# Optimization experiments

Hardware: AMD Instinct MI355X
Metric: run time of the kernel (lower is better)

Reference implementation:

```python
import jax, jax.numpy as jnp
import numpy as np

N_SCALES = 4
WINDOW = 64
REDUCTION = 4
EPS = 5e-05


def conv3x3_reflect(x, w):
    # reflect pad 1 then VALID 3x3 conv (no bias), NCHW/OIHW
    xp = jnp.pad(x, ((0, 0), (0, 0), (1, 1), (1, 1)), mode='reflect')
    return jax.lax.conv_general_dilated(
        xp, w, window_strides=(1, 1), padding='VALID',
        dimension_numbers=('NCHW', 'OIHW', 'NCHW'))


def add_adjacent_clusters(x):
    # x: (N, u, k, w, e); concat rolled-back and rolled-forward clusters on window axis
    x_back = jnp.roll(x, 1, axis=2)
    x_fwd = jnp.roll(x, -1, axis=2)
    return jnp.concatenate([x, x_back, x_fwd], axis=3)


def setup_inputs() -> dict:
    key = jax.random.key(0)
    ks = jax.random.split(key, 6)
    N, Cin, H, W = 2, 200, 128, 128
    inp = {
        'input': jax.random.normal(ks[0], (N, Cin, H, W), dtype=jnp.float32),
        'semantic_label': jax.random.randint(ks[1], (N, N_SCALES, H, W), 0, 32, dtype=jnp.int32),
        'Wx': jax.random.normal(ks[2], (Cin // REDUCTION, Cin, 3, 3), dtype=jnp.float32) * 0.02,
        'Wy': jax.random.normal(ks[3], (Cin, Cin, 1, 1), dtype=jnp.float32) * 0.02,
        'Wout': jax.random.normal(ks[4], (Cin, Cin * N_SCALES, 1, 1), dtype=jnp.float32) * 0.02,
        'bout': jax.random.normal(ks[5], (Cin,), dtype=jnp.float32) * 0.02,
    }
    return inp


def reference(input, semantic_label, Wx, Wy, Wout, bout):
    N, Cin, H, W = input.shape
    L = H * W
    C = Cin // REDUCTION  # 50

    # embeddings: (N, L, C) and (N, L, C*reduction)
    x_embed = conv3x3_reflect(input, Wx).reshape(N, C, L).transpose(0, 2, 1)
    y_embed = jnp.einsum('nchw,oc->nohw', input, Wy[:, :, 0, 0]).reshape(N, Cin, L).transpose(0, 2, 1)

    # semantic prior embed: per-scale offset of 100, flatten to (N, n_scales*L)
    offsets = (jnp.arange(N_SCALES, dtype=semantic_label.dtype) * 100)[None, :, None]
    sl = (semantic_label.reshape(N, N_SCALES, L) + offsets).reshape(N, -1)

    indices = jnp.argsort(sl, axis=-1)          # (N, n_scales*L)
    undo_sort = jnp.argsort(indices, axis=-1)
    mod_indices = indices % L

    x_sorted = jnp.take_along_axis(x_embed, mod_indices[:, :, None], axis=1)  # (N, 4L, C)
    y_sorted = jnp.take_along_axis(y_embed, mod_indices[:, :, None], axis=1)  # (N, 4L, 4C)

    # L chosen divisible by window_size -> padding == 0
    assert L % WINDOW == 0
    K = L // WINDOW
    x_cl = x_sorted.reshape(N, N_SCALES, K, WINDOW, C)
    y_cl = y_sorted.reshape(N, N_SCALES, K, WINDOW, C * REDUCTION)

    # F.normalize(p=2, dim=-1, eps=5e-5): x / max(||x||, eps)
    norm = jnp.linalg.norm(x_cl, axis=-1, keepdims=True)
    x_match = x_cl / jnp.maximum(norm, EPS)
    x_match = add_adjacent_clusters(x_match)    # (N, u, K, 3*W, C)
    y_adj = add_adjacent_clusters(y_cl)         # (N, u, K, 3*W, 4C)

    raw_weight = jnp.einsum('bukie,bukje->bukij', x_cl, x_match)  # (N,u,K,W,3W)
    weight = jax.nn.softmax(raw_weight, axis=-1)  # exp(raw - logsumexp)
    out = jnp.einsum('bukij,bukje->bukie', weight, y_adj)          # (N,u,K,W,4C)

    out = out.reshape(N, N_SCALES * L, C * REDUCTION)
    out = jnp.take_along_axis(out, undo_sort[:, :, None], axis=1)  # unsort
    out = out.reshape(N, N_SCALES, L, C * REDUCTION)
    out = out.transpose(0, 1, 3, 2).reshape(N, N_SCALES * C * REDUCTION, H, W)

    # 1x1 conv_out with bias + residual
    out = jnp.einsum('nchw,oc->nohw', out, Wout[:, :, 0, 0]) + bout[None, :, None, None]
    return out + input
```

## Files before the change

### kernel.cpp

```cpp
#include <hip/hip_runtime.h>
#include <hip/hip_bf16.h>
#include <math.h>

#define L      16384
#define CIN    200
#define CE     50
#define NS     4
#define KCL    256
#define WIN    64
#define NKEY   192

__global__ __launch_bounds__(256) void k_conv3(const float* __restrict__ in,
                                               const float* __restrict__ Wx,
                                               float* __restrict__ xe) {
  const int ocg  = blockIdx.x;
  const int tile = blockIdx.y;
  const int n    = blockIdx.z;
  const int th = tile >> 3, tw = tile & 7;
  const int ty = threadIdx.x >> 4, tx = threadIdx.x & 15;
  const int oc0 = ocg * 10;
  const int tid = threadIdx.x;

  __shared__ __align__(16) float patch[4 * 18 * 20];

  const float* inN = in + (size_t)n * CIN * L;
  const float* wB  = Wx + (size_t)oc0 * CIN * 9;

  int goff[6], loff[6];
#pragma unroll
  for (int j = 0; j < 6; ++j) {
    int idx = tid + j * 256;
    if (idx < 1296) {
      int ic = idx / 324, rem = idx % 324;
      int r = rem / 18, c = rem % 18;
      int gh = th * 16 + r - 1, gw = tw * 16 + c - 1;
      gh = gh < 0 ? -gh : (gh > 127 ? 254 - gh : gh);
      gw = gw < 0 ? -gw : (gw > 127 ? 254 - gw : gw);
      goff[j] = ic * L + gh * 128 + gw;
      loff[j] = ic * 360 + r * 20 + c;
    } else {
      goff[j] = -1;
      loff[j] = 0;
    }
  }

  float acc[10];
#pragma unroll
  for (int o = 0; o < 10; ++o) acc[o] = 0.f;

  float pf[6];
#pragma unroll
  for (int j = 0; j < 6; ++j) pf[j] = (goff[j] >= 0) ? inN[goff[j]] : 0.f;

  for (int s = 0; s < 50; ++s) {
    __syncthreads();
#pragma unroll
    for (int j = 0; j < 6; ++j)
      if (goff[j] >= 0) patch[loff[j]] = pf[j];
    __syncthreads();
    if (s < 49) {
      const float* src = inN + (size_t)(s + 1) * 4 * L;
#pragma unroll
      for (int j = 0; j < 6; ++j) pf[j] = (goff[j] >= 0) ? src[goff[j]] : 0.f;
    }

    float p[4][9];
#pragma unroll
    for (int icc = 0; icc < 4; ++icc) {
      const float* pb = &patch[icc * 360 + ty * 20 + tx];
#pragma unroll
      for (int dr = 0; dr < 3; ++dr)
#pragma unroll
        for (int dc = 0; dc < 3; ++dc)
          p[icc][dr * 3 + dc] = pb[dr * 20 + dc];
    }
    const float* wS = wB + (size_t)(4 * s) * 9;
#pragma unroll
    for (int o = 0; o < 10; ++o) {
      const float* wO = wS + (size_t)o * CIN * 9;
#pragma unroll
      for (int icc = 0; icc < 4; ++icc)
#pragma unroll
        for (int q = 0; q < 9; ++q)
          acc[o] = fmaf(p[icc][q], wO[icc * 9 + q], acc[o]);
    }
  }

  const int l = (th * 16 + ty) * 128 + (tw * 16 + tx);
  float* xrow = xe + ((size_t)n * L + l) * CE + oc0;
#pragma unroll
  for (int o = 0; o < 5; ++o)
    *(float2*)&xrow[o * 2] = make_float2(acc[o * 2], acc[o * 2 + 1]);
}

__global__ __launch_bounds__(256) void k_wy(const float* __restrict__ in,
                                            const float* __restrict__ Wy,
                                            float* __restrict__ ye) {
  const int n  = blockIdx.y;
  const int l0 = blockIdx.x * 64;
  __shared__ __align__(16) float At[20][64];
  __shared__ __align__(16) float Wt[20][208];
  const int pg = threadIdx.x >> 4, og = threadIdx.x & 15;

  float acc[4][13];
#pragma unroll
  for (int p = 0; p < 4; ++p)
#pragma unroll
    for (int j = 0; j < 13; ++j) acc[p][j] = 0.f;

  for (int idx = threadIdx.x; idx < 20 * 8; idx += 256)
    Wt[idx >> 3][200 + (idx & 7)] = 0.f;

  const float* inN = in + (size_t)n * CIN * L + l0;
  for (int c0 = 0; c0 < CIN; c0 += 20) {
    __syncthreads();
    for (int idx = threadIdx.x; idx < 20 * 64; idx += 256) {
      int k = idx >> 6, p = idx & 63;
      At[k][p] = inN[(size_t)(c0 + k) * L + p];
    }
    for (int idx = threadIdx.x; idx < 200 * 20; idx += 256) {
      int oc = idx / 20, k = idx % 20;
      Wt[k][oc] = Wy[(size_t)oc * CIN + c0 + k];
    }
    __syncthreads();
#pragma unroll
    for (int k = 0; k < 20; ++k) {
      float4 av = *(const float4*)&At[k][pg * 4];
      float a[4] = {av.x, av.y, av.z, av.w};
      float b[13];
#pragma unroll
      for (int j = 0; j < 13; ++j) b[j] = Wt[k][og * 13 + j];
#pragma unroll
      for (int p = 0; p < 4; ++p)
#pragma unroll
        for (int j = 0; j < 13; ++j) acc[p][j] = fmaf(a[p], b[j], acc[p][j]);
    }
  }
#pragma unroll
  for (int p = 0; p < 4; ++p) {
    int l = l0 + pg * 4 + p;
    float* yrow = ye + ((size_t)n * L + l) * CIN;
#pragma unroll
    for (int j = 0; j < 13; ++j) {
      int oc = og * 13 + j;
      if (oc < CIN) yrow[oc] = acc[p][j];
    }
  }
}

__global__ __launch_bounds__(256) void k_hist(const int* __restrict__ sl,
                                              int* __restrict__ hist) {
  const int blk = blockIdx.x;
  const int n = blk >> 7, ch = blk & 127;
  __shared__ int h[128];
  if (threadIdx.x < 128) h[threadIdx.x] = 0;
  __syncthreads();
#pragma unroll
  for (int it = 0; it < 2; ++it) {
    int pos = ch * 512 + it * 256 + threadIdx.x;
    int u = pos >> 14, l = pos & (L - 1);
    int lab = sl[((size_t)n * NS + u) * L + l] & 31;
    atomicAdd(&h[u * 32 + lab], 1);
  }
  __syncthreads();
  if (threadIdx.x < 128) hist[(blk << 7) + threadIdx.x] = h[threadIdx.x];
}

__global__ __launch_bounds__(128) void k_scan(const int* __restrict__ hist,
                                              int* __restrict__ offs) {
  const int n = blockIdx.x, b = threadIdx.x;
  __shared__ int tot[128];
  __shared__ int basebuf[128];
  int t = 0;
  for (int c = 0; c < 128; ++c) t += hist[(((size_t)n * 128 + c) << 7) + b];
  tot[b] = t;
  __syncthreads();
  if (b == 0) {
    int run = 0;
    for (int i = 0; i < 128; ++i) { basebuf[i] = run; run += tot[i]; }
  }
  __syncthreads();
  int run = basebuf[b];
  for (int c = 0; c < 128; ++c) {
    offs[(((size_t)n * 128 + c) << 7) + b] = run;
    run += hist[(((size_t)n * 128 + c) << 7) + b];
  }
}

__global__ __launch_bounds__(512) void k_scatter(const int* __restrict__ sl,
                                                 const int* __restrict__ offs,
                                                 int* __restrict__ perm) {
  const int blk = blockIdx.x;
  const int n = blk >> 7, ch = blk & 127;
  const int tid = threadIdx.x, wv = tid >> 6, lane = tid & 63;
  __shared__ int wh[8][128];
  for (int idx = tid; idx < 1024; idx += 512) ((int*)wh)[idx] = 0;
  __syncthreads();
  const int pos = ch * 512 + tid;
  const int u = pos >> 14, l = pos & (L - 1);
  const int b = u * 32 + (sl[((size_t)n * NS + u) * L + l] & 31);
  atomicAdd(&wh[wv][b], 1);
  int lr = 0;
  for (int s = 0; s < 64; ++s) {
    int ob = __shfl(b, s);
    lr += (s < lane && ob == b) ? 1 : 0;
  }
  __syncthreads();
  if (tid < 128) {
    int run = 0;
#pragma unroll
    for (int w = 0; w < 8; ++w) { int v = wh[w][tid]; wh[w][tid] = run; run += v; }
  }
  __syncthreads();
  const int rank = offs[(blk << 7) + b] + wh[wv][b] + lr;
  perm[(size_t)n * (NS * L) + rank] = pos;
}

#define PT_P  68
#define QS_P  68
#define KS_P  68
#define YT_P  100
#define EHC   100

__global__ __launch_bounds__(512) void k_attn(const float* __restrict__ xe,
                                              const float* __restrict__ ye,
                                              const int* __restrict__ perm,
                                              float* __restrict__ attnO) {
  const int kcl = blockIdx.x;
  const int u   = blockIdx.y;
  const int n   = blockIdx.z >> 1;
  const int eh  = blockIdx.z & 1;
  const int tid = threadIdx.x;

  __shared__ __align__(16) float Qst[CE * QS_P];
  __shared__ __align__(16) float Kst[CE * KS_P];
  __shared__ __align__(16) float Pt[WIN * PT_P];
  __shared__ __align__(16) float Yt[WIN * YT_P];
  __shared__ int   lidxS[NKEY];
  __shared__ float rmaxS[WIN];
  __shared__ float rsumS[WIN];
  __shared__ float facS[WIN];

  if (tid < NKEY) {
    int kj = tid < 64 ? kcl
           : (tid < 128 ? ((kcl + KCL - 1) & (KCL - 1)) : ((kcl + 1) & (KCL - 1)));
    int p = (u << 14) + (kj << 6) + (tid & 63);
    lidxS[tid] = perm[(size_t)n * (NS * L) + p] & (L - 1);
  }
  if (tid < WIN) { rmaxS[tid] = -1e30f; rsumS[tid] = 0.f; }
  __syncthreads();

  {
    const int j = tid >> 3, c8 = tid & 7;
    const float* xrow = xe + ((size_t)n * L + lidxS[j]) * CE;
#pragma unroll
    for (int k = 0; k < 7; ++k) {
      int c = c8 + 8 * k;
      if (c < CE) Qst[c * QS_P + j] = xrow[c];
    }
  }

  const int ig = tid >> 5, jg = tid & 31;
  const int i0 = ig * 4, j0 = jg * 2;
  const int rt = tid >> 6, lane = tid & 63;
  const int r0 = rt * 8, e0 = lane * 2;
  const bool pvact = lane < 50;

  float acc[8][2];
#pragma unroll
  for (int rr = 0; rr < 8; ++rr) { acc[rr][0] = 0.f; acc[rr][1] = 0.f; }

  const float* yeN = ye + (size_t)n * L * CIN + eh * EHC;

  for (int T = 0; T < 3; ++T) {
    const int jb = T * 64;
    if (T) __syncthreads();

    {
      const int j = tid >> 3, c8 = tid & 7;
      const float* xrow = xe + ((size_t)n * L + lidxS[jb + j]) * CE;
      float v[7];
      float ss = 0.f;
#pragma unroll
      for (int k = 0; k < 7; ++k) {
        int c = c8 + 8 * k;
        v[k] = (c < CE) ? xrow[c] : 0.f;
        ss = fmaf(v[k], v[k], ss);
      }
      ss += __shfl_xor(ss, 1); ss += __shfl_xor(ss, 2); ss += __shfl_xor(ss, 4);
      float inv = 1.f / fmaxf(sqrtf(ss), 5e-5f);
#pragma unroll
      for (int k = 0; k < 7; ++k) {
        int c = c8 + 8 * k;
        if (c < CE) Kst[c * KS_P + j] = v[k] * inv;
      }
    }
    for (int idx = tid; idx < WIN * 25; idx += 512) {
      int j = idx / 25, c = idx % 25;
      *(float4*)&Yt[j * YT_P + c * 4] =
          *(const float4*)&yeN[(size_t)lidxS[jb + j] * CIN + c * 4];
    }
    __syncthreads();

    {
      float s[4][2];
#pragma unroll
      for (int a = 0; a < 4; ++a) { s[a][0] = 0.f; s[a][1] = 0.f; }
      for (int c = 0; c < CE; ++c) {
        float4 qv = *(const float4*)&Qst[c * QS_P + i0];
        float2 kv = *(const float2*)&Kst[c * KS_P + j0];
        s[0][0] = fmaf(qv.x, kv.x, s[0][0]); s[0][1] = fmaf(qv.x, kv.y, s[0][1]);
        s[1][0] = fmaf(qv.y, kv.x, s[1][0]); s[1][1] = fmaf(qv.y, kv.y, s[1][1]);
        s[2][0] = fmaf(qv.z, kv.x, s[2][0]); s[2][1] = fmaf(qv.z, kv.y, s[2][1]);
        s[3][0] = fmaf(qv.w, kv.x, s[3][0]); s[3][1] = fmaf(qv.w, kv.y, s[3][1]);
      }
      float nm[4], fc[4], ts[4];
#pragma unroll
      for (int a = 0; a < 4; ++a) {
        float tm = fmaxf(s[a][0], s[a][1]);
        tm = fmaxf(tm, __shfl_xor(tm, 1));
        tm = fmaxf(tm, __shfl_xor(tm, 2));
        tm = fmaxf(tm, __shfl_xor(tm, 4));
        tm = fmaxf(tm, __shfl_xor(tm, 8));
        tm = fmaxf(tm, __shfl_xor(tm, 16));
        float mo = rmaxS[i0 + a];
        nm[a] = fmaxf(mo, tm);
        fc[a] = __expf(mo - nm[a]);
        s[a][0] = __expf(s[a][0] - nm[a]);
        s[a][1] = __expf(s[a][1] - nm[a]);
        float t = s[a][0] + s[a][1];
        t += __shfl_xor(t, 1); t += __shfl_xor(t, 2); t += __shfl_xor(t, 4);
        t += __shfl_xor(t, 8); t += __shfl_xor(t, 16);
        ts[a] = t;
      }
      *(float4*)&Pt[(j0 + 0) * PT_P + i0] =
          make_float4(s[0][0], s[1][0], s[2][0], s[3][0]);
      *(float4*)&Pt[(j0 + 1) * PT_P + i0] =
          make_float4(s[0][1], s[1][1], s[2][1], s[3][1]);
      if (jg == 0) {
#pragma unroll
        for (int a = 0; a < 4; ++a) {
          rmaxS[i0 + a] = nm[a];
          rsumS[i0 + a] = rsumS[i0 + a] * fc[a] + ts[a];
          facS[i0 + a]  = fc[a];
        }
      }
    }
    __syncthreads();

    if (pvact) {
      float f8[8];
#pragma unroll
      for (int rr = 0; rr < 8; ++rr) f8[rr] = facS[r0 + rr];
#pragma unroll
      for (int rr = 0; rr < 8; ++rr) { acc[rr][0] *= f8[rr]; acc[rr][1] *= f8[rr]; }
#pragma unroll 4
      for (int k = 0; k < WIN; ++k) {
        float4 pA = *(const float4*)&Pt[k * PT_P + r0];
        float4 pB = *(const float4*)&Pt[k * PT_P + r0 + 4];
        float2 yv = *(const float2*)&Yt[k * YT_P + e0];
        acc[0][0] = fmaf(pA.x, yv.x, acc[0][0]); acc[0][1] = fmaf(pA.x, yv.y, acc[0][1]);
        acc[1][0] = fmaf(pA.y, yv.x, acc[1][0]); acc[1][1] = fmaf(pA.y, yv.y, acc[1][1]);
        acc[2][0] = fmaf(pA.z, yv.x, acc[2][0]); acc[2][1] = fmaf(pA.z, yv.y, acc[2][1]);
        acc[3][0] = fmaf(pA.w, yv.x, acc[3][0]); acc[3][1] = fmaf(pA.w, yv.y, acc[3][1]);
        acc[4][0] = fmaf(pB.x, yv.x, acc[4][0]); acc[4][1] = fmaf(pB.x, yv.y, acc[4][1]);
        acc[5][0] = fmaf(pB.y, yv.x, acc[5][0]); acc[5][1] = fmaf(pB.y, yv.y, acc[5][1]);
        acc[6][0] = fmaf(pB.z, yv.x, acc[6][0]); acc[6][1] = fmaf(pB.z, yv.y, acc[6][1]);
        acc[7][0] = fmaf(pB.w, yv.x, acc[7][0]); acc[7][1] = fmaf(pB.w, yv.y, acc[7][1]);
      }
    }
  }

  if (pvact) {
#pragma unroll
    for (int rr = 0; rr < 8; ++rr) {
      float is = 1.f / rsumS[r0 + rr];
      float* orow = attnO + (((size_t)(n * NS + u) * L) + lidxS[r0 + rr]) * CIN
                  + eh * EHC + e0;
      *(float2*)orow = make_float2(acc[rr][0] * is, acc[rr][1] * is);
    }
  }
}

__global__ __launch_bounds__(256) void k_wout(const float* __restrict__ attnO,
                                              const float* __restrict__ Wo,
                                              const float* __restrict__ bo,
                                              const float* __restrict__ in,
                                              float* __restrict__ out) {
  const int n  = blockIdx.y;
  const int l0 = blockIdx.x * 64;
  __shared__ __align__(16) char sm[44160];
  float* At = (float*)sm;
  float* Wt = (float*)(sm + 10880);
  const int pg = threadIdx.x >> 4, og = threadIdx.x & 15;
  const int tid = threadIdx.x;

  float acc[4][13];
#pragma unroll
  for (int p = 0; p < 4; ++p)
#pragma unroll
    for (int j = 0; j < 13; ++j) acc[p][j] = 0.f;

  for (int idx = tid; idx < 40 * 8; idx += 256)
    Wt[(idx >> 3) * 208 + 200 + (idx & 7)] = 0.f;

  for (int c0 = 0; c0 < 800; c0 += 40) {
    const int u = c0 / 200, e0 = c0 % 200;
    __syncthreads();
    for (int idx = tid; idx < 64 * 40; idx += 256) {
      int p = idx / 40, kk = idx % 40;
      At[kk * 68 + p] = attnO[(((size_t)(n * NS + u) * L) + l0 + p) * CIN + e0 + kk];
    }
    for (int idx = tid; idx < 200 * 40; idx += 256) {
      int oc = idx / 40, kk = idx % 40;
      Wt[kk * 208 + oc] = Wo[(size_t)oc * 800 + c0 + kk];
    }
    __syncthreads();
#pragma unroll 8
    for (int kk = 0; kk < 40; ++kk) {
      float4 av = *(const float4*)&At[kk * 68 + pg * 4];
      float a[4] = {av.x, av.y, av.z, av.w};
      float b[13];
#pragma unroll
      for (int j = 0; j < 13; ++j) b[j] = Wt[kk * 208 + og * 13 + j];
#pragma unroll
      for (int p = 0; p < 4; ++p)
#pragma unroll
        for (int j = 0; j < 13; ++j) acc[p][j] = fmaf(a[p], b[j], acc[p][j]);
    }
  }
  __syncthreads();

  float* Ot = (float*)sm;
  for (int r = 0; r < 2; ++r) {
    const int ocb = r * 104;
    const int width = (r == 0) ? 104 : 96;
#pragma unroll
    for (int p = 0; p < 4; ++p)
#pragma unroll
      for (int j = 0; j < 13; ++j) {
        int oc = og * 13 + j;
        if (oc >= ocb && oc < ocb + width)
          Ot[(oc - ocb) * 64 + pg * 4 + p] = acc[p][j];
      }
    __syncthreads();
    for (int idx = tid; idx < width * 64; idx += 256) {
      int oc2 = idx >> 6, p = idx & 63;
      size_t o = ((size_t)n * CIN + ocb + oc2) * L + l0 + p;
      out[o] = Ot[oc2 * 64 + p] + bo[ocb + oc2] + in[o];
    }
    __syncthreads();
  }
}

extern "C" void kernel_launch(void* const* d_in, const int* in_sizes, int n_in,
                              void* d_out, int out_size, void* d_ws, size_t ws_size,
                              hipStream_t stream) {
  const float* in = (const float*)d_in[0];
  const int*   sl = (const int*)d_in[1];
  const float* Wx = (const float*)d_in[2];
  const float* Wy = (const float*)d_in[3];
  const float* Wo = (const float*)d_in[4];
  const float* bo = (const float*)d_in[5];
  float* out = (float*)d_out;

  float* xe   = (float*)d_ws;
  float* ye   = xe + (size_t)2 * L * CE;
  float* attn = ye + (size_t)2 * L * CIN;
  int*   perm = (int*)(attn + (size_t)2 * NS * L * CIN);
  int*   hist = perm + (size_t)2 * NS * L;
  int*   offs = hist + (size_t)2 * 128 * 128;

  k_conv3  <<<dim3(5, 64, 2),  256, 0, stream>>>(in, Wx, xe);
  k_wy     <<<dim3(256, 2),    256, 0, stream>>>(in, Wy, ye);
  k_hist   <<<256,             256, 0, stream>>>(sl, hist);
  k_scan   <<<2,               128, 0, stream>>>(hist, offs);
  k_scatter<<<256,             512, 0, stream>>>(sl, offs, perm);
  k_attn   <<<dim3(256, 4, 4), 512, 0, stream>>>(xe, ye, perm, attn);
  k_wout   <<<dim3(256, 2),    256, 0, stream>>>(attn, Wo, bo, in, out);
}
```

Before: 1.112 ms.

## Restructure 3x3 conv as split-K register-tiled GEMM with partial-sum reduction

Replaces the per-output-group direct conv with a kernel that tiles two image rows by all 50 output channels. Each thread holds a 4-pixel by 13-channel register tile, and weights and input rows are staged in shared memory in chunks of 10 channels. The 200 input channels are split four ways across blocks. Partial results go to a scratch buffer (aliasing the attention workspace) and a new reduction kernel sums them. This targets the low arithmetic intensity and redundant weight loads of the old kernel, at the cost of an extra launch and extra global traffic for the partial sums.

```diff
diff --git a/kernel.cpp b/kernel.cpp
--- a/kernel.cpp
+++ b/kernel.cpp
@@ -10,87 +10,105 @@
 #define WIN    64
 #define NKEY   192
 
-__global__ __launch_bounds__(256) void k_conv3(const float* __restrict__ in,
-                                               const float* __restrict__ Wx,
-                                               float* __restrict__ xe) {
-  const int ocg  = blockIdx.x;
-  const int tile = blockIdx.y;
-  const int n    = blockIdx.z;
-  const int th = tile >> 3, tw = tile & 7;
-  const int ty = threadIdx.x >> 4, tx = threadIdx.x & 15;
-  const int oc0 = ocg * 10;
+#define KC    10
+#define AT_S  132
+#define WT_S  64
+
+__global__ __launch_bounds__(256) void k_conv3p(const float* __restrict__ in,
+                                                const float* __restrict__ Wx,
+                                                float* __restrict__ xp) {
+  const int icg = blockIdx.x;
+  const int rp  = blockIdx.y;
+  const int n   = blockIdx.z;
   const int tid = threadIdx.x;
-
-  __shared__ __align__(16) float patch[4 * 18 * 20];
-
-  const float* inN = in + (size_t)n * CIN * L;
-  const float* wB  = Wx + (size_t)oc0 * CIN * 9;
-
-  int goff[6], loff[6];
-#pragma unroll
-  for (int j = 0; j < 6; ++j) {
-    int idx = tid + j * 256;
-    if (idx < 1296) {
-      int ic = idx / 324, rem = idx % 324;
-      int r = rem / 18, c = rem % 18;
-      int gh = th * 16 + r - 1, gw = tw * 16 + c - 1;
-      gh = gh < 0 ? -gh : (gh > 127 ? 254 - gh : gh);
-      gw = gw < 0 ? -gw : (gw > 127 ? 254 - gw : gw);
-      goff[j] = ic * L + gh * 128 + gw;
-      loff[j] = ic * 360 + r * 20 + c;
-    } else {
-      goff[j] = -1;
-      loff[j] = 0;
-    }
-  }
-
-  float acc[10];
-#pragma unroll
-  for (int o = 0; o < 10; ++o) acc[o] = 0.f;
-
-  float pf[6];
-#pragma unroll
-  for (int j = 0; j < 6; ++j) pf[j] = (goff[j] >= 0) ? inN[goff[j]] : 0.f;
-
-  for (int s = 0; s < 50; ++s) {
-    __syncthreads();
-#pragma unroll
-    for (int j = 0; j < 6; ++j)
-      if (goff[j] >= 0) patch[loff[j]] = pf[j];
-    __syncthreads();
-    if (s < 49) {
-      const float* src = inN + (size_t)(s + 1) * 4 * L;
-#pragma unroll
-      for (int j = 0; j < 6; ++j) pf[j] = (goff[j] >= 0) ? src[goff[j]] : 0.f;
-    }
-
-    float p[4][9];
-#pragma unroll
-    for (int icc = 0; icc < 4; ++icc) {
-      const float* pb = &patch[icc * 360 + ty * 20 + tx];
-#pragma unroll
-      for (int dr = 0; dr < 3; ++dr)
-#pragma unroll
-        for (int dc = 0; dc < 3; ++dc)
-          p[icc][dr * 3 + dc] = pb[dr * 20 + dc];
-    }
-    const float* wS = wB + (size_t)(4 * s) * 9;
-#pragma unroll
-    for (int o = 0; o < 10; ++o) {
-      const float* wO = wS + (size_t)o * CIN * 9;
-#pragma unroll
-      for (int icc = 0; icc < 4; ++icc)
-#pragma unroll
-        for (int q = 0; q < 9; ++q)
-          acc[o] = fmaf(p[icc][q], wO[icc * 9 + q], acc[o]);
-    }
-  }
-
-  const int l = (th * 16 + ty) * 128 + (tw * 16 + tx);
-  float* xrow = xe + ((size_t)n * L + l) * CE + oc0;
-#pragma unroll
-  for (int o = 0; o < 5; ++o)
-    *(float2*)&xrow[o * 2] = make_float2(acc[o * 2], acc[o * 2 + 1]);
+  const int ic0 = icg * 50;
+
+  __shared__ __align__(16) float At[KC * 4 * AT_S];
+  __shared__ __align__(16) float Wt[KC * 9 * WT_S];
+
+  const int pxg = tid & 63;
+  const int ocg = tid >> 6;
+  const int px4 = pxg * 4;
+  const int c0  = px4 & 127;
+  const int hr  = px4 >> 7;
+  const int oc0 = ocg * 13;
+  const int h0  = rp * 2;
+
+  float acc[4][13];
+#pragma unroll
+  for (int p = 0; p < 4; ++p)
+#pragma unroll
+    for (int j = 0; j < 13; ++j) acc[p][j] = 0.f;
+
+  const float* inN = in + ((size_t)n * CIN + ic0) * L;
+
+  for (int st = 0; st < 5; ++st) {
+    __syncthreads();
+    for (int idx = tid; idx < KC * 4 * 130; idx += 256) {
+      int k = idx / 520, rem = idx % 520;
+      int r = rem / 130, ci = rem % 130;
+      int gr = h0 - 1 + r; gr = gr < 0 ? -gr : (gr > 127 ? 254 - gr : gr);
+      int gc = ci - 1;     gc = gc < 0 ? -gc : (gc > 127 ? 254 - gc : gc);
+      At[(k * 4 + r) * AT_S + ci] = inN[(size_t)(st * KC + k) * L + gr * 128 + gc];
+    }
+    for (int idx = tid; idx < KC * 9 * 52; idx += 256) {
+      int k = idx / 468, rem = idx % 468;
+      int q = rem / 52, s = rem % 52;
+      int og = s / 13, j = s % 13;
+      Wt[(k * 9 + q) * WT_S + og * 16 + j] =
+          Wx[(size_t)(og * 13 + j) * (CIN * 9) + (size_t)(ic0 + st * KC + k) * 9 + q];
+    }
+    __syncthreads();
+
+    for (int k = 0; k < KC; ++k) {
+      float v[3][6];
+#pragma unroll
+      for (int dr = 0; dr < 3; ++dr) {
+        const float* ar = &At[(k * 4 + hr + dr) * AT_S + c0];
+        float4 a4 = *(const float4*)ar;
+        float2 a2 = *(const float2*)(ar + 4);
+        v[dr][0] = a4.x; v[dr][1] = a4.y; v[dr][2] = a4.z;
+        v[dr][3] = a4.w; v[dr][4] = a2.x; v[dr][5] = a2.y;
+      }
+      const float* wk = &Wt[k * 9 * WT_S + ocg * 16];
+#pragma unroll
+      for (int q = 0; q < 9; ++q) {
+        const int dr = q / 3, dc = q % 3;
+        float4 w0 = *(const float4*)&wk[q * WT_S + 0];
+        float4 w1 = *(const float4*)&wk[q * WT_S + 4];
+        float4 w2 = *(const float4*)&wk[q * WT_S + 8];
+        float  wc = wk[q * WT_S + 12];
+        float w[13] = {w0.x, w0.y, w0.z, w0.w, w1.x, w1.y, w1.z, w1.w,
+                       w2.x, w2.y, w2.z, w2.w, wc};
+#pragma unroll
+        for (int j = 0; j < 13; ++j)
+#pragma unroll
+          for (int p = 0; p < 4; ++p)
+            acc[p][j] = fmaf(v[dr][p + dc], w[j], acc[p][j]);
+      }
+    }
+  }
+
+  float* xpN = xp + (size_t)(icg * 2 + n) * L * CE;
+#pragma unroll
+  for (int p = 0; p < 4; ++p) {
+    float* row = xpN + (size_t)(rp * 256 + px4 + p) * CE + oc0;
+#pragma unroll
+    for (int j = 0; j < 13; ++j)
+      if (oc0 + j < CE) row[j] = acc[p][j];
+  }
+}
+
+__global__ __launch_bounds__(256) void k_cred(const float* __restrict__ xp,
+                                              float* __restrict__ xe) {
+  const int tot4 = 2 * L * CE / 4;
+  int i = blockIdx.x * 256 + threadIdx.x;
+  if (i < tot4) {
+    const float4* p = (const float4*)xp;
+    float4 a = p[i], b = p[tot4 + i], c = p[2 * tot4 + i], d = p[3 * tot4 + i];
+    ((float4*)xe)[i] = make_float4(a.x + b.x + c.x + d.x, a.y + b.y + c.y + d.y,
+                                   a.z + b.z + c.z + d.z, a.w + b.w + c.w + d.w);
+  }
 }
 
 __global__ __launch_bounds__(256) void k_wy(const float* __restrict__ in,
@@ -470,8 +488,10 @@
   int*   perm = (int*)(attn + (size_t)2 * NS * L * CIN);
   int*   hist = perm + (size_t)2 * NS * L;
   int*   offs = hist + (size_t)2 * 128 * 128;
-
-  k_conv3  <<<dim3(5, 64, 2),  256, 0, stream>>>(in, Wx, xe);
+  float* xpart = attn;
+
+  k_conv3p <<<dim3(4, 64, 2),  256, 0, stream>>>(in, Wx, xpart);
+  k_cred   <<<1600,            256, 0, stream>>>(xpart, xe);
   k_wy     <<<dim3(256, 2),    256, 0, stream>>>(in, Wy, ye);
   k_hist   <<<256,             256, 0, stream>>>(sl, hist);
   k_scan   <<<2,               128, 0, stream>>>(hist, offs);
```

New measurement: 974.2 us. -12.4%, faster.
